# Kernel tuning notes

Hardware: AMD Instinct MI355X
Metric: run time of the kernel (lower is better)

Reference implementation:

```python
import jax, jax.numpy as jnp
import numpy as np

B, S, D = 64, 1024, 800      # batch, seq_len, encoder hidden (2*hidden_dim, bidirectional)
MS, T = 16, 32               # max slots (spans) per sample, max span length
H = 200                      # LSTM hidden per direction = trs_hidden_dim // 2
NS = 12                      # number of slot names in the domain


def setup_inputs() -> dict:
    key = jax.random.key(0)
    ks = jax.random.split(key, 13)
    s = 0.05
    return {
        "hidden_layers": jax.random.normal(ks[0], (B, S, D), jnp.float32),
        "Wih_f": jax.random.normal(ks[1], (4 * H, D), jnp.float32) * s,
        "Whh_f": jax.random.normal(ks[2], (4 * H, H), jnp.float32) * s,
        "bih_f": jax.random.normal(ks[3], (4 * H,), jnp.float32) * s,
        "bhh_f": jax.random.normal(ks[4], (4 * H,), jnp.float32) * s,
        "Wih_b": jax.random.normal(ks[5], (4 * H, D), jnp.float32) * s,
        "Whh_b": jax.random.normal(ks[6], (4 * H, H), jnp.float32) * s,
        "bih_b": jax.random.normal(ks[7], (4 * H,), jnp.float32) * s,
        "bhh_b": jax.random.normal(ks[8], (4 * H,), jnp.float32) * s,
        "slot_embs": jax.random.normal(ks[9], (2 * H, NS), jnp.float32) * s,
        "span_starts": jnp.sort(jax.random.randint(ks[10], (B, MS), 0, S - T), axis=-1),
        "span_lens": jax.random.randint(ks[11], (B, MS), 1, T + 1),
        "slot_mask": jnp.ones((B, MS), jnp.float32),
    }


def _lstm_scan(x, m, Wih, Whh, bih, bhh):
    """Masked unidirectional LSTM. x: [N,T,Din], m: [N,T] bool-ish. Returns [N,T,H]."""
    N = x.shape[0]
    bias = bih + bhh

    def step(carry, xm):
        h, c = carry
        xt, mt = xm
        z = xt @ Wih.T + h @ Whh.T + bias            # [N, 4H], PyTorch gate order i,f,g,o
        i, f, g, o = jnp.split(z, 4, axis=-1)
        c_new = jax.nn.sigmoid(f) * c + jax.nn.sigmoid(i) * jnp.tanh(g)
        h_new = jax.nn.sigmoid(o) * jnp.tanh(c_new)
        mm = mt[:, None]
        h = jnp.where(mm, h_new, h)                  # freeze state on padded steps
        c = jnp.where(mm, c_new, c)
        return (h, c), h

    h0 = jnp.zeros((N, H), x.dtype)
    (_, _), hs = jax.lax.scan(step, (h0, h0), (jnp.swapaxes(x, 0, 1), m.T.astype(bool)))
    return jnp.swapaxes(hs, 0, 1)


def reference(hidden_layers, Wih_f, Whh_f, bih_f, bhh_f, Wih_b, Whh_b, bih_b, bhh_b,
              slot_embs, span_starts, span_lens, slot_mask):
    Bv, Sv, Dv = hidden_layers.shape
    # Padded ragged span gather: [B, MS, T]
    idx = jnp.clip(span_starts[..., None] + jnp.arange(T), 0, Sv - 1)
    tok_mask = (jnp.arange(T)[None, None, :] < span_lens[..., None]).astype(hidden_layers.dtype)
    spans = hidden_layers[jnp.arange(Bv)[:, None, None], idx]      # [B, MS, T, D]

    x = spans.reshape(Bv * MS, T, Dv)
    m = tok_mask.reshape(Bv * MS, T)
    h_f = _lstm_scan(x, m, Wih_f, Whh_f, bih_f, bhh_f)             # forward direction
    h_b = _lstm_scan(x[:, ::-1], m[:, ::-1], Wih_b, Whh_b, bih_b, bhh_b)[:, ::-1]
    y = jnp.concatenate([h_f, h_b], axis=-1)                       # [N, T, 2H]

    feats = jnp.sum(y * m[..., None], axis=1).reshape(Bv, MS, 2 * H)  # sum over span tokens
    logits = jnp.einsum('bmh,hn->bmn', feats, slot_embs)           # slot-name scores
    return logits * slot_mask[..., None]
```

## Files before the change

kernel.cpp:

```cpp
#include <hip/hip_runtime.h>


typedef __attribute__((ext_vector_type(4))) float f32x4;
typedef __attribute__((ext_vector_type(8))) short s16x8;

__device__ __forceinline__ unsigned short f2bf(float f) {
    union { float f; unsigned int u; } a; a.f = f;
    unsigned int u = a.u;
    u += 0x7fffu + ((u >> 16) & 1u);
    return (unsigned short)(u >> 16);
}
__device__ __forceinline__ float bf2f(unsigned short s) {
    union { unsigned int u; float f; } a; a.u = ((unsigned int)s) << 16; return a.f;
}
__device__ __forceinline__ void async_copy16(const void* g, void* l) {
    __builtin_amdgcn_global_load_lds(
        (const __attribute__((address_space(1))) unsigned int*)g,
        (__attribute__((address_space(3))) unsigned int*)l, 16, 0, 0);
}
__device__ __forceinline__ float sigf_(float x) {
    return 1.f / (1.f + __expf(-x));
}
__device__ __forceinline__ float tanhf_(float x) {
    float ax = fabsf(x);
    float e = __expf(-2.f * ax);
    float r = (1.f - e) / (1.f + e);
    return x < 0.f ? -r : r;
}

__global__ void pack_kernel(const float* __restrict__ Wih_f, const float* __restrict__ Wih_b,
                            const float* __restrict__ Whh_f, const float* __restrict__ Whh_b,
                            const float* __restrict__ bih_f, const float* __restrict__ bhh_f,
                            const float* __restrict__ bih_b, const float* __restrict__ bhh_b,
                            unsigned short* __restrict__ Wp, unsigned short* __restrict__ WhhP,
                            float* __restrict__ biasP)
{
    int tid = blockIdx.x * blockDim.x + threadIdx.x;
    if (tid < 1664 * 800) {
        int n = tid / 800, k = tid - n * 800;
        float v = 0.f;
        if (n < 800)       v = Wih_f[n * 800 + k];
        else if (n < 1600) v = Wih_b[(n - 800) * 800 + k];
        Wp[tid] = f2bf(v);
        return;
    }
    int t2 = tid - 1664 * 800;
    if (t2 < 1600 * 224) {
        int n = t2 / 224, k = t2 - n * 224;
        float v = 0.f;
        if (k < 200) v = (n < 800) ? Whh_f[n * 200 + k] : Whh_b[(n - 800) * 200 + k];
        WhhP[t2] = f2bf(v);
        return;
    }
    int t3 = t2 - 1600 * 224;
    if (t3 < 1664) {
        float v = 0.f;
        if (t3 < 800)       v = bih_f[t3] + bhh_f[t3];
        else if (t3 < 1600) v = bih_b[t3 - 800] + bhh_b[t3 - 800];
        biasP[t3] = v;
    }
}

__global__ void gather_kernel(const float* __restrict__ hidden, const int* __restrict__ starts,
                              unsigned short* __restrict__ Xg)
{
    int tid = blockIdx.x * blockDim.x + threadIdx.x;
    if (tid >= 32768 * 200) return;
    int row = tid / 200;
    int c4  = tid - row * 200;
    int t   = row >> 10, seq = row & 1023;
    int b   = seq >> 4;
    int src = starts[seq] + t;
    src = src < 1023 ? src : 1023;
    const float4 v = *(const float4*)(hidden + (size_t)(b * 1024 + src) * 800 + c4 * 4);
    ushort4 o;
    o.x = f2bf(v.x); o.y = f2bf(v.y); o.z = f2bf(v.z); o.w = f2bf(v.w);
    *(ushort4*)(Xg + (size_t)row * 800 + c4 * 4) = o;
}

__global__ __launch_bounds__(256) void gemm_kernel(const unsigned short* __restrict__ Xg,
                                                   const unsigned short* __restrict__ Wp,
                                                   const float* __restrict__ biasP,
                                                   unsigned short* __restrict__ Zf,
                                                   unsigned short* __restrict__ Zb)
{
    __shared__ __align__(16) unsigned short As[128 * 32];
    __shared__ __align__(16) unsigned short Bs[128 * 32];
    const int tid = threadIdx.x;
    const int wid = tid >> 6, lane = tid & 63;
    const int m0 = blockIdx.x * 128;
    const int n0 = blockIdx.y * 128;
    const int wm = (wid >> 1) * 64, wn = (wid & 1) * 64;
    const int l15 = lane & 15, l4 = lane >> 4;

    f32x4 acc[4][4];
#pragma unroll
    for (int i = 0; i < 4; i++)
#pragma unroll
        for (int j = 0; j < 4; j++) acc[i][j] = (f32x4){0.f, 0.f, 0.f, 0.f};

    const int r0 = tid >> 2,         kc0 = (tid & 3) * 8;
    const int r1 = (256 + tid) >> 2, kc1 = (tid & 3) * 8;
    unsigned short* AsB0 = As + (size_t)(wid * 64) * 8;
    unsigned short* AsB1 = As + (size_t)(256 + wid * 64) * 8;
    unsigned short* BsB0 = Bs + (size_t)(wid * 64) * 8;
    unsigned short* BsB1 = Bs + (size_t)(256 + wid * 64) * 8;

    for (int kb = 0; kb < 25; ++kb) {
        const int kk = kb * 32;
        async_copy16(Xg + (size_t)(m0 + r0) * 800 + kk + kc0, AsB0);
        async_copy16(Xg + (size_t)(m0 + r1) * 800 + kk + kc1, AsB1);
        async_copy16(Wp + (size_t)(n0 + r0) * 800 + kk + kc0, BsB0);
        async_copy16(Wp + (size_t)(n0 + r1) * 800 + kk + kc1, BsB1);
        __syncthreads();

        s16x8 a[4], b[4];
#pragma unroll
        for (int i = 0; i < 4; i++)
            a[i] = *(const s16x8*)(As + (wm + i * 16 + l15) * 32 + l4 * 8);
#pragma unroll
        for (int i = 0; i < 4; i++)
            b[i] = *(const s16x8*)(Bs + (wn + i * 16 + l15) * 32 + l4 * 8);
#pragma unroll
        for (int im = 0; im < 4; im++)
#pragma unroll
            for (int in = 0; in < 4; in++)
                acc[im][in] = __builtin_amdgcn_mfma_f32_16x16x32_bf16(a[im], b[in], acc[im][in], 0, 0, 0);
        __syncthreads();
    }

    float bias_v[4];
#pragma unroll
    for (int in = 0; in < 4; in++) bias_v[in] = biasP[n0 + wn + in * 16 + l15];

#pragma unroll
    for (int im = 0; im < 4; im++) {
        int mbase = m0 + wm + im * 16 + l4 * 4;
#pragma unroll
        for (int in = 0; in < 4; in++) {
            int col = n0 + wn + in * 16 + l15;
            if (col < 1600) {
                int d = col >= 800;
                int u = col - d * 800;
                unsigned short* Zd = d ? Zb : Zf;
#pragma unroll
                for (int r = 0; r < 4; r++)
                    Zd[(size_t)(mbase + r) * 832 + u] = f2bf(acc[im][in][r] + bias_v[in]);
            }
        }
    }
}

__global__ __launch_bounds__(512, 2) void lstm_kernel(const unsigned short* __restrict__ Zf,
                                                      const unsigned short* __restrict__ Zb,
                                                      const unsigned short* __restrict__ WhhP,
                                                      const int* __restrict__ span_lens,
                                                      float* __restrict__ feats)
{
    __shared__ __align__(16) unsigned short h_lds[16 * 232];
    __shared__ __align__(16) unsigned short zbuf[2][16 * 832];
    __shared__ __align__(16) float zm[16 * 816];

    const int bx = blockIdx.x;
    const int dir = bx >> 6;
    const int g = bx & 63;
    const int tid = threadIdx.x;
    const int w = tid >> 6, lane = tid & 63;
    const int l15 = lane & 15, l4 = lane >> 4;
    const unsigned short* __restrict__ Zd = dir ? Zb : Zf;

    s16x8 breg[3][7];
#pragma unroll
    for (int rt = 0; rt < 3; ++rt) {
        const int colg = dir * 800 + (w * 3 + rt) * 16 + l15;
        const unsigned short* wrow = WhhP + (size_t)colg * 224 + l4 * 8;
#pragma unroll
        for (int kk = 0; kk < 7; ++kk)
            breg[rt][kk] = *(const s16x8*)(wrow + kk * 32);
    }

    for (int i = tid; i < 16 * 232; i += 512) h_lds[i] = 0;

    f32x4 c_st[2], f_st[2];
    int s_g[2], u4_g[2], len_g[2], valid[2];
#pragma unroll
    for (int q = 0; q < 2; ++q) {
        c_st[q] = (f32x4){0.f, 0.f, 0.f, 0.f};
        f_st[q] = (f32x4){0.f, 0.f, 0.f, 0.f};
        int grp = tid + q * 512;
        valid[q] = (grp < 800);
        int s = valid[q] ? (grp / 50) : 0;
        int u4 = valid[q] ? (grp - s * 50) : 0;
        s_g[q] = s; u4_g[q] = u4;
        len_g[q] = valid[q] ? span_lens[g * 16 + s] : -1;
    }

    {
        const int t0 = dir ? 31 : 0;
        const unsigned short* gb = Zd + (size_t)(t0 * 1024 + g * 16) * 832;
        for (int c = w; c < 26; c += 8)
            async_copy16(gb + c * 512 + lane * 8, (unsigned short*)zbuf[0] + c * 512);
    }
    __syncthreads();

    for (int step = 0; step < 32; ++step) {
        const int t = dir ? (31 - step) : step;
        const int cur = step & 1, nxt = cur ^ 1;
        if (step < 31) {
            const int tn = dir ? (t - 1) : (t + 1);
            const unsigned short* gb = Zd + (size_t)(tn * 1024 + g * 16) * 832;
            for (int c = w; c < 26; c += 8)
                async_copy16(gb + c * 512 + lane * 8, (unsigned short*)zbuf[nxt] + c * 512);
        }

        s16x8 afr[7];
        {
            const unsigned short* hrow = h_lds + l15 * 232 + l4 * 8;
#pragma unroll
            for (int kk = 0; kk < 7; ++kk)
                afr[kk] = *(const s16x8*)(hrow + kk * 32);
        }
#pragma unroll
        for (int rt = 0; rt < 3; ++rt) {
            f32x4 acc = (f32x4){0.f, 0.f, 0.f, 0.f};
#pragma unroll
            for (int kk = 0; kk < 7; ++kk)
                acc = __builtin_amdgcn_mfma_f32_16x16x32_bf16(afr[kk], breg[rt][kk], acc, 0, 0, 0);
            const int col = (w * 3 + rt) * 16 + l15;
#pragma unroll
            for (int r = 0; r < 4; ++r)
                zm[(l4 * 4 + r) * 816 + col] = acc[r];
        }
        for (int j = 24 + w; j < 50; j += 8) {
            const int colg = dir * 800 + j * 16 + l15;
            const unsigned short* wrow = WhhP + (size_t)colg * 224 + l4 * 8;
            s16x8 bs[7];
#pragma unroll
            for (int kk = 0; kk < 7; ++kk)
                bs[kk] = *(const s16x8*)(wrow + kk * 32);
            f32x4 acc = (f32x4){0.f, 0.f, 0.f, 0.f};
#pragma unroll
            for (int kk = 0; kk < 7; ++kk)
                acc = __builtin_amdgcn_mfma_f32_16x16x32_bf16(afr[kk], bs[kk], acc, 0, 0, 0);
#pragma unroll
            for (int r = 0; r < 4; ++r)
                zm[(l4 * 4 + r) * 816 + j * 16 + l15] = acc[r];
        }
        __syncthreads();

#pragma unroll
        for (int q = 0; q < 2; ++q) {
            if (valid[q] && t < len_g[q]) {
                const int s = s_g[q], u4 = u4_g[q];
                const float* zr = zm + s * 816 + u4 * 4;
                f32x4 zi = *(const f32x4*)(zr);
                f32x4 zf = *(const f32x4*)(zr + 200);
                f32x4 zg = *(const f32x4*)(zr + 400);
                f32x4 zo = *(const f32x4*)(zr + 600);
                const unsigned short* zb = zbuf[cur] + s * 832 + u4 * 4;
                ushort4 bi = *(const ushort4*)(zb);
                ushort4 bf = *(const ushort4*)(zb + 200);
                ushort4 bg = *(const ushort4*)(zb + 400);
                ushort4 bo = *(const ushort4*)(zb + 600);
                zi[0] += bf2f(bi.x); zi[1] += bf2f(bi.y); zi[2] += bf2f(bi.z); zi[3] += bf2f(bi.w);
                zf[0] += bf2f(bf.x); zf[1] += bf2f(bf.y); zf[2] += bf2f(bf.z); zf[3] += bf2f(bf.w);
                zg[0] += bf2f(bg.x); zg[1] += bf2f(bg.y); zg[2] += bf2f(bg.z); zg[3] += bf2f(bg.w);
                zo[0] += bf2f(bo.x); zo[1] += bf2f(bo.y); zo[2] += bf2f(bo.z); zo[3] += bf2f(bo.w);
                f32x4 cn, hn;
#pragma unroll
                for (int r = 0; r < 4; ++r) {
                    cn[r] = sigf_(zf[r]) * c_st[q][r] + sigf_(zi[r]) * tanhf_(zg[r]);
                    hn[r] = sigf_(zo[r]) * tanhf_(cn[r]);
                }
                c_st[q] = cn;
                f_st[q] += hn;
                ushort4 hp;
                hp.x = f2bf(hn[0]); hp.y = f2bf(hn[1]); hp.z = f2bf(hn[2]); hp.w = f2bf(hn[3]);
                *(ushort4*)(h_lds + s * 232 + u4 * 4) = hp;
            }
        }
        __syncthreads();
    }

#pragma unroll
    for (int q = 0; q < 2; ++q) {
        if (valid[q]) {
            float* fp = feats + (size_t)(g * 16 + s_g[q]) * 400 + dir * 200 + u4_g[q] * 4;
            *(f32x4*)fp = f_st[q];
        }
    }
}

__global__ void logits_kernel(const float* __restrict__ feats, const float* __restrict__ se,
                              const float* __restrict__ slot_mask, float* __restrict__ out)
{
    int tid = blockIdx.x * blockDim.x + threadIdx.x;
    if (tid >= 1024 * 12) return;
    int n = tid / 12, ns = tid - n * 12;
    const float* f = feats + (size_t)n * 400;
    float acc = 0.f;
    for (int u = 0; u < 400; ++u) acc += f[u] * se[u * 12 + ns];
    out[tid] = acc * slot_mask[n];
}

extern "C" void kernel_launch(void* const* d_in, const int* in_sizes, int n_in,
                              void* d_out, int out_size, void* d_ws, size_t ws_size,
                              hipStream_t stream)
{
    const float* hidden      = (const float*)d_in[0];
    const float* Wih_f       = (const float*)d_in[1];
    const float* Whh_f       = (const float*)d_in[2];
    const float* bih_f       = (const float*)d_in[3];
    const float* bhh_f       = (const float*)d_in[4];
    const float* Wih_b       = (const float*)d_in[5];
    const float* Whh_b       = (const float*)d_in[6];
    const float* bih_b       = (const float*)d_in[7];
    const float* bhh_b       = (const float*)d_in[8];
    const float* slot_embs   = (const float*)d_in[9];
    const int*   span_starts = (const int*)d_in[10];
    const int*   span_lens   = (const int*)d_in[11];
    const float* slot_mask   = (const float*)d_in[12];
    float* out = (float*)d_out;

    char* ws = (char*)d_ws;
    unsigned short* Xg    = (unsigned short*)(ws + 0);
    unsigned short* Wp    = (unsigned short*)(ws + 52428800);
    unsigned short* WhhP  = (unsigned short*)(ws + 55091200);
    float*          biasP = (float*)         (ws + 55808000);
    unsigned short* Zf    = (unsigned short*)(ws + 55814656);
    unsigned short* Zb    = (unsigned short*)(ws + 110340608);
    float*          feats = (float*)         (ws + 164866560);

    {
        int total = 1664 * 800 + 1600 * 224 + 1664;
        int blocks = (total + 255) / 256;
        pack_kernel<<<blocks, 256, 0, stream>>>(Wih_f, Wih_b, Whh_f, Whh_b,
                                                bih_f, bhh_f, bih_b, bhh_b,
                                                Wp, WhhP, biasP);
    }
    gather_kernel<<<25600, 256, 0, stream>>>(hidden, span_starts, Xg);
    gemm_kernel<<<dim3(256, 13), 256, 0, stream>>>(Xg, Wp, biasP, Zf, Zb);
    lstm_kernel<<<128, 512, 0, stream>>>(Zf, Zb, WhhP, span_lens, feats);
    logits_kernel<<<48, 256, 0, stream>>>(feats, slot_embs, slot_mask, out);
}
```

Before: 641.4 us.

## Interleave LSTM gates per unit and fuse cell update into MFMA registers

Repacks the recurrent weights so each 16-unit tile holds all four gates, and has the GEMM write Z with gates interleaved per hidden unit. The LSTM kernel can then apply the cell update straight from MFMA accumulators, with no fp32 zm staging round-trip through LDS and one barrier per step instead of two. It also double-buffers h and halves the sequences per block (8 valid rows in 16-row MFMA tiles) to launch 256 blocks, which fills more CUs. The cost is wasted MFMA rows and more Whh reloads from global each step.

New measurement: 792.7 us. 23.6% more time.

```diff
diff --git a/kernel.cpp b/kernel.cpp
--- a/kernel.cpp
+++ b/kernel.cpp
@@ -32,7 +32,7 @@
                             const float* __restrict__ Whh_f, const float* __restrict__ Whh_b,
                             const float* __restrict__ bih_f, const float* __restrict__ bhh_f,
                             const float* __restrict__ bih_b, const float* __restrict__ bhh_b,
-                            unsigned short* __restrict__ Wp, unsigned short* __restrict__ WhhP,
+                            unsigned short* __restrict__ Wp, unsigned short* __restrict__ WhhP2,
                             float* __restrict__ biasP)
 {
     int tid = blockIdx.x * blockDim.x + threadIdx.x;
@@ -45,14 +45,19 @@
         return;
     }
     int t2 = tid - 1664 * 800;
-    if (t2 < 1600 * 224) {
-        int n = t2 / 224, k = t2 - n * 224;
+    if (t2 < 1664 * 224) {
+        int row = t2 / 224, k = t2 - row * 224;
+        int d = row >= 832;
+        int rg = row - d * 832;
+        int gate = rg / 208;
+        int u = rg - gate * 208;
         float v = 0.f;
-        if (k < 200) v = (n < 800) ? Whh_f[n * 200 + k] : Whh_b[(n - 800) * 200 + k];
-        WhhP[t2] = f2bf(v);
+        if (u < 200 && k < 200)
+            v = (d ? Whh_b : Whh_f)[(gate * 200 + u) * 200 + k];
+        WhhP2[t2] = f2bf(v);
         return;
     }
-    int t3 = t2 - 1600 * 224;
+    int t3 = t2 - 1664 * 224;
     if (t3 < 1664) {
         float v = 0.f;
         if (t3 < 800)       v = bih_f[t3] + bhh_f[t3];
@@ -141,64 +146,72 @@
             int col = n0 + wn + in * 16 + l15;
             if (col < 1600) {
                 int d = col >= 800;
-                int u = col - d * 800;
+                int cg = col - d * 800;
+                int gate = (cg >= 600) ? 3 : (cg >= 400) ? 2 : (cg >= 200) ? 1 : 0;
+                int u = cg - gate * 200;
+                int zcol = u * 4 + gate;
                 unsigned short* Zd = d ? Zb : Zf;
 #pragma unroll
                 for (int r = 0; r < 4; r++)
-                    Zd[(size_t)(mbase + r) * 832 + u] = f2bf(acc[im][in][r] + bias_v[in]);
-            }
-        }
-    }
-}
-
-__global__ __launch_bounds__(512, 2) void lstm_kernel(const unsigned short* __restrict__ Zf,
+                    Zd[(size_t)(mbase + r) * 832 + zcol] = f2bf(acc[im][in][r] + bias_v[in]);
+            }
+        }
+    }
+}
+
+__global__ __launch_bounds__(256, 1) void lstm_kernel(const unsigned short* __restrict__ Zf,
                                                       const unsigned short* __restrict__ Zb,
-                                                      const unsigned short* __restrict__ WhhP,
+                                                      const unsigned short* __restrict__ WhhP2,
                                                       const int* __restrict__ span_lens,
                                                       float* __restrict__ feats)
 {
-    __shared__ __align__(16) unsigned short h_lds[16 * 232];
-    __shared__ __align__(16) unsigned short zbuf[2][16 * 832];
-    __shared__ __align__(16) float zm[16 * 816];
+    __shared__ __align__(16) unsigned short h2[2][16 * 232];
+    __shared__ __align__(16) unsigned short zbuf[2][8 * 832];
 
     const int bx = blockIdx.x;
-    const int dir = bx >> 6;
-    const int g = bx & 63;
+    const int dir = bx >> 7;
+    const int g8 = bx & 127;
+    const int seq0 = g8 * 8;
     const int tid = threadIdx.x;
     const int w = tid >> 6, lane = tid & 63;
     const int l15 = lane & 15, l4 = lane >> 4;
     const unsigned short* __restrict__ Zd = dir ? Zb : Zf;
 
-    s16x8 breg[3][7];
-#pragma unroll
-    for (int rt = 0; rt < 3; ++rt) {
-        const int colg = dir * 800 + (w * 3 + rt) * 16 + l15;
-        const unsigned short* wrow = WhhP + (size_t)colg * 224 + l4 * 8;
-#pragma unroll
-        for (int kk = 0; kk < 7; ++kk)
-            breg[rt][kk] = *(const s16x8*)(wrow + kk * 32);
-    }
-
-    for (int i = tid; i < 16 * 232; i += 512) h_lds[i] = 0;
-
-    f32x4 c_st[2], f_st[2];
-    int s_g[2], u4_g[2], len_g[2], valid[2];
-#pragma unroll
-    for (int q = 0; q < 2; ++q) {
-        c_st[q] = (f32x4){0.f, 0.f, 0.f, 0.f};
-        f_st[q] = (f32x4){0.f, 0.f, 0.f, 0.f};
-        int grp = tid + q * 512;
-        valid[q] = (grp < 800);
-        int s = valid[q] ? (grp / 50) : 0;
-        int u4 = valid[q] ? (grp - s * 50) : 0;
-        s_g[q] = s; u4_g[q] = u4;
-        len_g[q] = valid[q] ? span_lens[g * 16 + s] : -1;
+    for (int i = tid; i < 2 * 16 * 232; i += 256) ((unsigned short*)h2)[i] = 0;
+
+    s16x8 breg[2][4][7];
+#pragma unroll
+    for (int q = 0; q < 2; ++q)
+#pragma unroll
+        for (int gate = 0; gate < 4; ++gate) {
+            const int row = dir * 832 + gate * 208 + (q * 4 + w) * 16 + l15;
+            const unsigned short* wp = WhhP2 + (size_t)row * 224 + l4 * 8;
+#pragma unroll
+            for (int kk = 0; kk < 7; ++kk)
+                breg[q][gate][kk] = *(const s16x8*)(wp + kk * 32);
+        }
+    const int ut2 = 8 + w;
+
+    f32x4 cst[4], fst[4];
+    unsigned short hr[4][4];
+#pragma unroll
+    for (int q = 0; q < 4; ++q) {
+        cst[q] = (f32x4){0.f, 0.f, 0.f, 0.f};
+        fst[q] = (f32x4){0.f, 0.f, 0.f, 0.f};
+#pragma unroll
+        for (int r = 0; r < 4; ++r) hr[q][r] = 0;
+    }
+    int len4[4];
+    {
+        int sbase = (l4 < 2 ? l4 : 1) * 4;
+#pragma unroll
+        for (int r = 0; r < 4; ++r) len4[r] = span_lens[seq0 + sbase + r];
     }
 
     {
         const int t0 = dir ? 31 : 0;
-        const unsigned short* gb = Zd + (size_t)(t0 * 1024 + g * 16) * 832;
-        for (int c = w; c < 26; c += 8)
+        const unsigned short* gb = Zd + (size_t)(t0 * 1024 + seq0) * 832;
+        for (int c = w; c < 13; c += 4)
             async_copy16(gb + c * 512 + lane * 8, (unsigned short*)zbuf[0] + c * 512);
     }
     __syncthreads();
@@ -208,85 +221,110 @@
         const int cur = step & 1, nxt = cur ^ 1;
         if (step < 31) {
             const int tn = dir ? (t - 1) : (t + 1);
-            const unsigned short* gb = Zd + (size_t)(tn * 1024 + g * 16) * 832;
-            for (int c = w; c < 26; c += 8)
+            const unsigned short* gb = Zd + (size_t)(tn * 1024 + seq0) * 832;
+            for (int c = w; c < 13; c += 4)
                 async_copy16(gb + c * 512 + lane * 8, (unsigned short*)zbuf[nxt] + c * 512);
         }
 
         s16x8 afr[7];
         {
-            const unsigned short* hrow = h_lds + l15 * 232 + l4 * 8;
+            const unsigned short* hrow = h2[cur] + l15 * 232 + l4 * 8;
 #pragma unroll
             for (int kk = 0; kk < 7; ++kk)
                 afr[kk] = *(const s16x8*)(hrow + kk * 32);
         }
-#pragma unroll
-        for (int rt = 0; rt < 3; ++rt) {
-            f32x4 acc = (f32x4){0.f, 0.f, 0.f, 0.f};
+        f32x4 accA[2][4];
+#pragma unroll
+        for (int q = 0; q < 2; ++q)
+#pragma unroll
+            for (int gate = 0; gate < 4; ++gate) {
+                f32x4 a = (f32x4){0.f, 0.f, 0.f, 0.f};
+#pragma unroll
+                for (int kk = 0; kk < 7; ++kk)
+                    a = __builtin_amdgcn_mfma_f32_16x16x32_bf16(afr[kk], breg[q][gate][kk], a, 0, 0, 0);
+                accA[q][gate] = a;
+            }
+        f32x4 accS[4];
+#pragma unroll
+        for (int gate = 0; gate < 4; ++gate) {
+            const int row = dir * 832 + gate * 208 + ut2 * 16 + l15;
+            const unsigned short* wp = WhhP2 + (size_t)row * 224 + l4 * 8;
+            s16x8 bs[7];
 #pragma unroll
             for (int kk = 0; kk < 7; ++kk)
-                acc = __builtin_amdgcn_mfma_f32_16x16x32_bf16(afr[kk], breg[rt][kk], acc, 0, 0, 0);
-            const int col = (w * 3 + rt) * 16 + l15;
-#pragma unroll
-            for (int r = 0; r < 4; ++r)
-                zm[(l4 * 4 + r) * 816 + col] = acc[r];
-        }
-        for (int j = 24 + w; j < 50; j += 8) {
-            const int colg = dir * 800 + j * 16 + l15;
-            const unsigned short* wrow = WhhP + (size_t)colg * 224 + l4 * 8;
-            s16x8 bs[7];
+                bs[kk] = *(const s16x8*)(wp + kk * 32);
+            f32x4 a = (f32x4){0.f, 0.f, 0.f, 0.f};
 #pragma unroll
             for (int kk = 0; kk < 7; ++kk)
-                bs[kk] = *(const s16x8*)(wrow + kk * 32);
-            f32x4 acc = (f32x4){0.f, 0.f, 0.f, 0.f};
-#pragma unroll
-            for (int kk = 0; kk < 7; ++kk)
-                acc = __builtin_amdgcn_mfma_f32_16x16x32_bf16(afr[kk], bs[kk], acc, 0, 0, 0);
-#pragma unroll
-            for (int r = 0; r < 4; ++r)
-                zm[(l4 * 4 + r) * 816 + j * 16 + l15] = acc[r];
+                a = __builtin_amdgcn_mfma_f32_16x16x32_bf16(afr[kk], bs[kk], a, 0, 0, 0);
+            accS[gate] = a;
+        }
+        f32x4 acc12[4];
+        if (w == 3) {
+#pragma unroll
+            for (int gate = 0; gate < 4; ++gate) {
+                const int row = dir * 832 + gate * 208 + 12 * 16 + l15;
+                const unsigned short* wp = WhhP2 + (size_t)row * 224 + l4 * 8;
+                s16x8 bs[7];
+#pragma unroll
+                for (int kk = 0; kk < 7; ++kk)
+                    bs[kk] = *(const s16x8*)(wp + kk * 32);
+                f32x4 a = (f32x4){0.f, 0.f, 0.f, 0.f};
+#pragma unroll
+                for (int kk = 0; kk < 7; ++kk)
+                    a = __builtin_amdgcn_mfma_f32_16x16x32_bf16(afr[kk], bs[kk], a, 0, 0, 0);
+                acc12[gate] = a;
+            }
+        }
+
+        if (l4 < 2) {
+            const unsigned short* zc = zbuf[cur];
+            unsigned short* h2n = h2[nxt];
+#pragma unroll
+            for (int qq = 0; qq < 4; ++qq) {
+                if (qq == 3 && w != 3) continue;
+                const int ut = (qq == 0) ? (0 * 4 + w) : (qq == 1) ? (1 * 4 + w)
+                             : (qq == 2) ? ut2 : 12;
+                const f32x4* ag = (qq == 0) ? accA[0] : (qq == 1) ? accA[1]
+                                : (qq == 2) ? accS : acc12;
+                const int ucol = ut * 16 + l15;
+#pragma unroll
+                for (int r = 0; r < 4; ++r) {
+                    const int s = l4 * 4 + r;
+                    const int live = (t < len4[r]);
+                    ushort4 zb4 = *(const ushort4*)(zc + s * 832 + ucol * 4);
+                    float zi = ag[0][r] + bf2f(zb4.x);
+                    float zf = ag[1][r] + bf2f(zb4.y);
+                    float zg = ag[2][r] + bf2f(zb4.z);
+                    float zo = ag[3][r] + bf2f(zb4.w);
+                    float cn = sigf_(zf) * cst[qq][r] + sigf_(zi) * tanhf_(zg);
+                    float hn = sigf_(zo) * tanhf_(cn);
+                    if (live) {
+                        cst[qq][r] = cn;
+                        fst[qq][r] += hn;
+                        hr[qq][r] = f2bf(hn);
+                    }
+                    h2n[s * 232 + ucol] = hr[qq][r];
+                }
+            }
         }
         __syncthreads();
-
-#pragma unroll
-        for (int q = 0; q < 2; ++q) {
-            if (valid[q] && t < len_g[q]) {
-                const int s = s_g[q], u4 = u4_g[q];
-                const float* zr = zm + s * 816 + u4 * 4;
-                f32x4 zi = *(const f32x4*)(zr);
-                f32x4 zf = *(const f32x4*)(zr + 200);
-                f32x4 zg = *(const f32x4*)(zr + 400);
-                f32x4 zo = *(const f32x4*)(zr + 600);
-                const unsigned short* zb = zbuf[cur] + s * 832 + u4 * 4;
-                ushort4 bi = *(const ushort4*)(zb);
-                ushort4 bf = *(const ushort4*)(zb + 200);
-                ushort4 bg = *(const ushort4*)(zb + 400);
-                ushort4 bo = *(const ushort4*)(zb + 600);
-                zi[0] += bf2f(bi.x); zi[1] += bf2f(bi.y); zi[2] += bf2f(bi.z); zi[3] += bf2f(bi.w);
-                zf[0] += bf2f(bf.x); zf[1] += bf2f(bf.y); zf[2] += bf2f(bf.z); zf[3] += bf2f(bf.w);
-                zg[0] += bf2f(bg.x); zg[1] += bf2f(bg.y); zg[2] += bf2f(bg.z); zg[3] += bf2f(bg.w);
-                zo[0] += bf2f(bo.x); zo[1] += bf2f(bo.y); zo[2] += bf2f(bo.z); zo[3] += bf2f(bo.w);
-                f32x4 cn, hn;
+    }
+
+    if (l4 < 2) {
+#pragma unroll
+        for (int qq = 0; qq < 4; ++qq) {
+            if (qq == 3 && w != 3) continue;
+            const int ut = (qq == 0) ? (0 * 4 + w) : (qq == 1) ? (1 * 4 + w)
+                         : (qq == 2) ? ut2 : 12;
+            const int u = ut * 16 + l15;
+            if (u < 200) {
 #pragma unroll
                 for (int r = 0; r < 4; ++r) {
-                    cn[r] = sigf_(zf[r]) * c_st[q][r] + sigf_(zi[r]) * tanhf_(zg[r]);
-                    hn[r] = sigf_(zo[r]) * tanhf_(cn[r]);
+                    const int s = l4 * 4 + r;
+                    feats[(size_t)(seq0 + s) * 400 + dir * 200 + u] = fst[qq][r];
                 }
-                c_st[q] = cn;
-                f_st[q] += hn;
-                ushort4 hp;
-                hp.x = f2bf(hn[0]); hp.y = f2bf(hn[1]); hp.z = f2bf(hn[2]); hp.w = f2bf(hn[3]);
-                *(ushort4*)(h_lds + s * 232 + u4 * 4) = hp;
-            }
-        }
-        __syncthreads();
-    }
-
-#pragma unroll
-    for (int q = 0; q < 2; ++q) {
-        if (valid[q]) {
-            float* fp = feats + (size_t)(g * 16 + s_g[q]) * 400 + dir * 200 + u4_g[q] * 4;
-            *(f32x4*)fp = f_st[q];
+            }
         }
     }
 }
@@ -323,23 +361,23 @@
     float* out = (float*)d_out;
 
     char* ws = (char*)d_ws;
-    unsigned short* Xg    = (unsigned short*)(ws + 0);
-    unsigned short* Wp    = (unsigned short*)(ws + 52428800);
-    unsigned short* WhhP  = (unsigned short*)(ws + 55091200);
-    float*          biasP = (float*)         (ws + 55808000);
-    unsigned short* Zf    = (unsigned short*)(ws + 55814656);
-    unsigned short* Zb    = (unsigned short*)(ws + 110340608);
-    float*          feats = (float*)         (ws + 164866560);
+    unsigned short* Xg     = (unsigned short*)(ws + 0);
+    unsigned short* Wp     = (unsigned short*)(ws + 52428800);
+    unsigned short* WhhP2  = (unsigned short*)(ws + 55091200);
+    float*          biasP  = (float*)         (ws + 55836672);
+    unsigned short* Zf     = (unsigned short*)(ws + 55843328);
+    unsigned short* Zb     = (unsigned short*)(ws + 110369280);
+    float*          feats  = (float*)         (ws + 164895232);
 
     {
-        int total = 1664 * 800 + 1600 * 224 + 1664;
+        int total = 1664 * 800 + 1664 * 224 + 1664;
         int blocks = (total + 255) / 256;
         pack_kernel<<<blocks, 256, 0, stream>>>(Wih_f, Wih_b, Whh_f, Whh_b,
                                                 bih_f, bhh_f, bih_b, bhh_b,
-                                                Wp, WhhP, biasP);
+                                                Wp, WhhP2, biasP);
     }
     gather_kernel<<<25600, 256, 0, stream>>>(hidden, span_starts, Xg);
     gemm_kernel<<<dim3(256, 13), 256, 0, stream>>>(Xg, Wp, biasP, Zf, Zb);
-    lstm_kernel<<<128, 512, 0, stream>>>(Zf, Zb, WhhP, span_lens, feats);
+    lstm_kernel<<<256, 256, 0, stream>>>(Zf, Zb, WhhP2, span_lens, feats);
     logits_kernel<<<48, 256, 0, stream>>>(feats, slot_embs, slot_mask, out);
 }
```
